# Performance work log

Measured on AMD Instinct MI355X. Metric: run time of the kernel, lower is better.

The kernel has to match this reference:

```python
import jax, jax.numpy as jnp
import numpy as np

C = 512        # num_channels
HEADS = 8      # num_channels // num_head_channels
DH = 64        # num_head_channels
G = 32         # num_groups
EPS = 1e-5
SCALE = DH ** -0.25  # pre-multiplied into q and k (scale applied twice -> 1/sqrt(DH))


def setup_inputs() -> dict:
    key = jax.random.key(0)
    ks = jax.random.split(key, 10)
    B, H, W = 2, 64, 64
    def w(k):
        return jax.random.normal(k, (C, C), jnp.float32) * 0.02
    def b(k):
        return jax.random.normal(k, (C,), jnp.float32) * 0.02
    return {
        "x": jax.random.normal(ks[0], (B, C, H, W), jnp.float32),
        "gn_w": jnp.ones((C,), jnp.float32),
        "gn_b": jnp.zeros((C,), jnp.float32),
        "wq": w(ks[1]), "bq": b(ks[2]),
        "wk": w(ks[3]), "bk": b(ks[4]),
        "wv": w(ks[5]), "bv": b(ks[6]),
        "wp": w(ks[7]), "bp": b(ks[8]),
    }


def reference(x, gn_w, gn_b, wq, bq, wk, bk, wv, bv, wp, bp):
    B, Cc, H, W = x.shape
    # GroupNorm over (C/G, H, W) per group
    xr = x.reshape(B, G, Cc // G, H * W)
    mean = xr.mean(axis=(2, 3), keepdims=True)
    var = xr.var(axis=(2, 3), keepdims=True)
    h = ((xr - mean) * jax.lax.rsqrt(var + EPS)).reshape(B, Cc, H, W)
    h = h * gn_w[None, :, None, None] + gn_b[None, :, None, None]
    # B C H W -> B (H W) C
    t = h.reshape(B, Cc, H * W).transpose(0, 2, 1)
    # q/k pre-multiplied by SCALE (equivalent to pre_multiply_weights_by_scale)
    q = (t @ wq.T + bq) * SCALE
    k = (t @ wk.T + bk) * SCALE
    v = t @ wv.T + bv
    def split_heads(a):  # B HW (h d) -> B h HW d
        return a.reshape(B, H * W, HEADS, DH).transpose(0, 2, 1, 3)
    q, k, v = split_heads(q), split_heads(k), split_heads(v)
    # full HWxHW score matrix, softmax over keys
    attn = jax.nn.softmax(jnp.einsum('bhqd,bhkd->bhqk', q, k), axis=-1)
    o = jnp.einsum('bhqk,bhkd->bhqd', attn, v)
    o = o.transpose(0, 2, 1, 3).reshape(B, H * W, Cc)  # join heads
    o = o @ wp.T + bp
    # B (H W) C -> B C H W, residual
    return o.transpose(0, 2, 1).reshape(B, Cc, H, W) + x
```

## Files before the change

### kernel.cpp

```cpp
#include <hip/hip_runtime.h>

#define HWN 4096
#define CCH 512
#define NHEAD 8
#define DHD 64
#define NBATCH 2
#define QK_SCALE 0.35355339059327373f
#define LOG2E    1.4426950408889634f

using floatx4 = __attribute__((ext_vector_type(4))) float;
using bf16x8  = __attribute__((ext_vector_type(8))) short;
using bf16x4  = __attribute__((ext_vector_type(4))) short;

__device__ __forceinline__ unsigned short f2b(float f) {
  union { float f; unsigned u; } x; x.f = f;
  unsigned r = x.u + 0x7FFFu + ((x.u >> 16) & 1u);
  return (unsigned short)(r >> 16);
}

__device__ __forceinline__ float b2f(unsigned short u) {
  union { unsigned u; float f; } x; x.u = ((unsigned)u) << 16;
  return x.f;
}

__device__ __forceinline__ float fast_exp2(float x) {
#if __has_builtin(__builtin_amdgcn_exp2f)
  return __builtin_amdgcn_exp2f(x);
#else
  return __expf(x * 0.69314718056f);
#endif
}

__device__ __forceinline__ unsigned pack_bf16_trunc(float lo, float hi) {
  return __builtin_amdgcn_perm(__float_as_uint(hi), __float_as_uint(lo), 0x07060302u);
}

__global__ __launch_bounds__(256) void prep_gn(
    const float* __restrict__ x, float* __restrict__ stat,
    const float* __restrict__ wq, const float* __restrict__ wk,
    const float* __restrict__ wv, const float* __restrict__ wp,
    const float* __restrict__ bq, const float* __restrict__ bk,
    const float* __restrict__ bv,
    unsigned short* __restrict__ Wqkv, unsigned short* __restrict__ Wp,
    float* __restrict__ bqkv) {
  if (blockIdx.x >= 4103) {
    int idx = blockIdx.x - 4103;
    int bg = idx & 63, part = idx >> 6;
    const float4* p = (const float4*)(x + (size_t)bg * 65536) + part * 2048;
    float s = 0.f, ss = 0.f;
    for (int i = threadIdx.x; i < 2048; i += 256) {
      float4 v = p[i];
      s  += v.x + v.y + v.z + v.w;
      ss += v.x*v.x + v.y*v.y + v.z*v.z + v.w*v.w;
    }
    for (int off = 32; off; off >>= 1) {
      s  += __shfl_xor(s, off);
      ss += __shfl_xor(ss, off);
    }
    __shared__ float red[8];
    int w = threadIdx.x >> 6;
    if ((threadIdx.x & 63) == 0) { red[w] = s; red[4 + w] = ss; }
    __syncthreads();
    if (threadIdx.x == 0) {
      float S  = red[0] + red[1] + red[2] + red[3];
      float SS = red[4] + red[5] + red[6] + red[7];
      atomicAdd(&stat[bg], S);
      atomicAdd(&stat[64 + bg], SS);
    }
    return;
  }
  int i = blockIdx.x * 256 + threadIdx.x;
  if (i < 786432) {
    int row = i >> 9;
    float v;
    if (row < 512)       v = wq[i] * (QK_SCALE * LOG2E);
    else if (row < 1024) v = wk[i - 262144] * QK_SCALE;
    else                 v = wv[i - 524288];
    Wqkv[i] = f2b(v);
  } else if (i < 1048576) {
    Wp[i - 786432] = f2b(wp[i - 786432]);
  } else if (i < 1050112) {
    int j = i - 1048576;
    float v = (j < 512) ? bq[j] * (QK_SCALE * LOG2E)
            : (j < 1024) ? bk[j - 512] * QK_SCALE
            : bv[j - 1024];
    bqkv[j] = v;
  }
}

__global__ __launch_bounds__(256) void gn_apply(
    const float* __restrict__ x, const float* __restrict__ stat,
    const float* __restrict__ gnw, const float* __restrict__ gnb,
    unsigned short* __restrict__ t) {
  int pt = blockIdx.x & 63;
  int ct = (blockIdx.x >> 6) & 7;
  int b  = blockIdx.x >> 9;
  int c0 = ct * 64, p0 = pt * 64;
  __shared__ float tile[64][68];
  int tid = threadIdx.x;
  for (int pp = 0; pp < 4; ++pp) {
    int f = (pp * 256 + tid) * 4;
    int cl = f >> 6, pl = f & 63;
    int c = c0 + cl;
    float4 v = *(const float4*)(x + ((size_t)(b * 512 + c)) * 4096 + p0 + pl);
    int g = c >> 4;
    float S    = stat[b * 32 + g];
    float SS   = stat[64 + b * 32 + g];
    float mean = S * (1.f / 65536.f);
    float var  = SS * (1.f / 65536.f) - mean * mean;
    float rstd = rsqrtf(var + 1e-5f);
    float w  = gnw[c] * rstd;
    float bb = gnb[c] - mean * w;
    tile[cl][pl + 0] = v.x * w + bb;
    tile[cl][pl + 1] = v.y * w + bb;
    tile[cl][pl + 2] = v.z * w + bb;
    tile[cl][pl + 3] = v.w * w + bb;
  }
  __syncthreads();
  for (int pp = 0; pp < 2; ++pp) {
    int f = (pp * 256 + tid) * 8;
    int pl = f >> 6, cl = f & 63;
    unsigned short u[8];
#pragma unroll
    for (int j = 0; j < 8; ++j) u[j] = f2b(tile[cl + j][pl]);
    *(uint4*)(t + ((size_t)(b * 4096 + p0 + pl)) * 512 + c0 + cl) = *(uint4*)u;
  }
}

__global__ __launch_bounds__(256) void gemm_qkv(
    const unsigned short* __restrict__ t, const unsigned short* __restrict__ Wqkv,
    const float* __restrict__ bqkv,
    unsigned short* __restrict__ qo, unsigned short* __restrict__ Kp,
    unsigned short* __restrict__ vo) {
  int M0 = blockIdx.x * 64;
  int N0 = blockIdx.y * 64;
  __shared__ unsigned short At[64][72];
  __shared__ unsigned short Bt[64][72];
  int tid = threadIdx.x, w = tid >> 6, l = tid & 63;
  int quad = l >> 4, m16 = l & 15;
  floatx4 acc[4] = {};
  for (int k0 = 0; k0 < 512; k0 += 64) {
    __syncthreads();
#pragma unroll
    for (int pp = 0; pp < 2; ++pp) {
      int f = (pp * 256 + tid) * 8;
      int r = f >> 6, c = f & 63;
      *(uint4*)&At[r][c] = *(const uint4*)(t    + (size_t)(M0 + r) * 512 + k0 + c);
      *(uint4*)&Bt[r][c] = *(const uint4*)(Wqkv + (size_t)(N0 + r) * 512 + k0 + c);
    }
    __syncthreads();
    bf16x8 af0 = *(const bf16x8*)&At[w * 16 + m16][quad * 8];
    bf16x8 af1 = *(const bf16x8*)&At[w * 16 + m16][32 + quad * 8];
#pragma unroll
    for (int nt = 0; nt < 4; ++nt) {
      bf16x8 b0 = *(const bf16x8*)&Bt[nt * 16 + m16][quad * 8];
      bf16x8 b1 = *(const bf16x8*)&Bt[nt * 16 + m16][32 + quad * 8];
      acc[nt] = __builtin_amdgcn_mfma_f32_16x16x32_bf16(af0, b0, acc[nt], 0, 0, 0);
      acc[nt] = __builtin_amdgcn_mfma_f32_16x16x32_bf16(af1, b1, acc[nt], 0, 0, 0);
    }
  }
  int which = N0 >> 9;
  int head  = (N0 & 511) >> 6;
  if (which == 2) {
    __syncthreads();
#pragma unroll
    for (int nt = 0; nt < 4; ++nt) {
      int d = nt * 16 + m16;
      float bias = bqkv[N0 + d];
#pragma unroll
      for (int r = 0; r < 4; ++r)
        At[d][w * 16 + quad * 4 + r] = f2b(acc[nt][r] + bias);
    }
    __syncthreads();
    int bb = M0 >> 12, p0 = M0 & 4095;
    unsigned short* dst = vo + ((size_t)(bb * 8 + head) * 64) * 4096;
#pragma unroll
    for (int pp = 0; pp < 2; ++pp) {
      int f = (pp * 256 + tid) * 8;
      int d = f >> 6, pl = f & 63;
      *(uint4*)(dst + (size_t)d * 4096 + p0 + pl) = *(uint4*)&At[d][pl];
    }
  } else if (which == 1) {
    __syncthreads();
#pragma unroll
    for (int nt = 0; nt < 4; ++nt) {
      float bias = bqkv[N0 + nt * 16 + m16];
#pragma unroll
      for (int r = 0; r < 4; ++r)
        At[w * 16 + quad * 4 + r][nt * 16 + m16] = f2b(acc[nt][r] + bias);
    }
    __syncthreads();
    int bb = M0 >> 12, p = M0 & 4095;
    int kb = p >> 7, halfblk = (p >> 6) & 1;
    int ig = halfblk * 4 + w;
    int ntl = w >> 1, hh = w & 1;
    int row = ntl * 32 + hh * 4 + ((m16 >> 2) << 3) + (m16 & 3);
    size_t dstb = (((size_t)(bb * 8 + head) * 32 + kb) * 8 + ig) * 1024;
#pragma unroll
    for (int pp = 0; pp < 2; ++pp)
      *(uint4*)(Kp + dstb + pp * 512 + l * 8) = *(uint4*)&At[row][pp * 32 + quad * 8];
  } else {
#pragma unroll
    for (int nt = 0; nt < 4; ++nt) {
      int n = N0 + nt * 16 + m16;
      float bias = bqkv[n];
      int d = n & 63;
#pragma unroll
      for (int r = 0; r < 4; ++r) {
        int m = M0 + w * 16 + quad * 4 + r;
        int b = m >> 12, pp2 = m & 4095;
        qo[(((size_t)(b * 8 + head) * 4096 + pp2) << 6) + d] = f2b(acc[nt][r] + bias);
      }
    }
  }
}

__global__ __launch_bounds__(256, 4) void attn(
    const unsigned short* __restrict__ q, const unsigned short* __restrict__ Kp,
    const unsigned short* __restrict__ vt,
    unsigned short* __restrict__ ob) {
  int qt = blockIdx.x;
  int bh = blockIdx.y;
  __shared__ unsigned short Klds[8192];
  __shared__ unsigned short Vt[64][128];
  int tid = threadIdx.x, w = tid >> 6, l = tid & 63;
  int quad = l >> 4, m16 = l & 15;
  const size_t vbase = (size_t)bh * HWN * DHD;

  int goff[4];
#pragma unroll
  for (int i = 0; i < 4; ++i) {
    int c = w * 4 + i;
    int row = 4 * c + (l >> 4);
    int cbl = l & 15;
    goff[i] = row * 4096 + ((cbl ^ (row & 15)) << 3);
  }

  bf16x8 qf0, qf1;
  {
    int qrow = qt * 64 + w * 16 + m16;
    const unsigned short* qp = q + vbase + (size_t)qrow * 64 + quad * 8;
    qf0 = *(const bf16x8*)qp;
    qf1 = *(const bf16x8*)(qp + 32);
  }
  bf16x8 ones;
#pragma unroll
  for (int z = 0; z < 8; ++z) ones[z] = (short)0x3F80;

  floatx4 accO[4] = {};
  floatx4 accL = {};
  float mrow = -1e30f;

  for (int kt = 0; kt < 32; ++kt) {
    __syncthreads();
    const unsigned short* kpb = Kp + (((size_t)bh * 32 + kt) * 8) * 1024;
    const unsigned short* vtile = vt + vbase + kt * 128;
#pragma unroll
    for (int i = 0; i < 4; ++i) {
      int c = w * 4 + i;
      __builtin_amdgcn_global_load_lds(
          (const __attribute__((address_space(1))) unsigned int*)(kpb + c * 512 + l * 8),
          (__attribute__((address_space(3))) unsigned int*)(Klds + c * 512),
          16, 0, 0);
      __builtin_amdgcn_global_load_lds(
          (const __attribute__((address_space(1))) unsigned int*)(vtile + goff[i]),
          (__attribute__((address_space(3))) unsigned int*)(&Vt[0][0] + c * 512),
          16, 0, 0);
    }
    __syncthreads();
    const unsigned short* kl = Klds + l * 8;
    floatx4 s[8];
#pragma unroll
    for (int ig = 0; ig < 8; ++ig) {
      bf16x8 kf0 = *(const bf16x8*)(kl + ig * 1024);
      bf16x8 kf1 = *(const bf16x8*)(kl + ig * 1024 + 512);
      floatx4 z = {};
      z = __builtin_amdgcn_mfma_f32_16x16x32_bf16(kf0, qf0, z, 0, 0, 0);
      s[ig] = __builtin_amdgcn_mfma_f32_16x16x32_bf16(kf1, qf1, z, 0, 0, 0);
    }
    float mx = s[0][0];
#pragma unroll
    for (int ig = 0; ig < 8; ++ig)
#pragma unroll
      for (int i = 0; i < 4; ++i) mx = fmaxf(mx, s[ig][i]);
    mx = fmaxf(mx, __shfl_xor(mx, 16));
    mx = fmaxf(mx, __shfl_xor(mx, 32));
    bool grew = mx > mrow + 8.0f;
    if (__ballot(grew)) {
      float mnew = grew ? mx : mrow;
      float alpha = fast_exp2(mrow - mnew);
      float al0 = __shfl(alpha, quad * 4 + 0);
      float al1 = __shfl(alpha, quad * 4 + 1);
      float al2 = __shfl(alpha, quad * 4 + 2);
      float al3 = __shfl(alpha, quad * 4 + 3);
#pragma unroll
      for (int dt = 0; dt < 4; ++dt) {
        accO[dt][0] *= al0; accO[dt][1] *= al1;
        accO[dt][2] *= al2; accO[dt][3] *= al3;
      }
      accL[0] *= al0; accL[1] *= al1; accL[2] *= al2; accL[3] *= al3;
      mrow = mnew;
    }
#pragma unroll
    for (int ig = 0; ig < 8; ++ig)
#pragma unroll
      for (int i = 0; i < 4; ++i)
        s[ig][i] = fast_exp2(s[ig][i] - mrow);
    bf16x8 pf[4];
#pragma unroll
    for (int nt = 0; nt < 4; ++nt) {
      union { unsigned u[4]; bf16x8 v; } pu;
      pu.u[0] = pack_bf16_trunc(s[nt * 2][0],     s[nt * 2][1]);
      pu.u[1] = pack_bf16_trunc(s[nt * 2][2],     s[nt * 2][3]);
      pu.u[2] = pack_bf16_trunc(s[nt * 2 + 1][0], s[nt * 2 + 1][1]);
      pu.u[3] = pack_bf16_trunc(s[nt * 2 + 1][2], s[nt * 2 + 1][3]);
      pf[nt] = pu.v;
    }
#pragma unroll
    for (int dt = 0; dt < 4; ++dt) {
#pragma unroll
      for (int nt = 0; nt < 4; ++nt) {
        bf16x8 vf = *(const bf16x8*)&Vt[dt * 16 + m16][((nt * 4 + quad) ^ m16) << 3];
        accO[dt] = __builtin_amdgcn_mfma_f32_16x16x32_bf16(pf[nt], vf, accO[dt], 0, 0, 0);
      }
    }
#pragma unroll
    for (int nt = 0; nt < 4; ++nt)
      accL = __builtin_amdgcn_mfma_f32_16x16x32_bf16(pf[nt], ones, accL, 0, 0, 0);
  }
  int b = bh >> 3, h = bh & 7;
  float li0 = 1.f / accL[0];
  float li1 = 1.f / accL[1];
  float li2 = 1.f / accL[2];
  float li3 = 1.f / accL[3];
  int qrow = qt * 64 + w * 16 + quad * 4;
  unsigned short* op = ob + ((size_t)(b * 4096 + qrow)) * 512 + h * 64;
#pragma unroll
  for (int dt = 0; dt < 4; ++dt) {
    int d = dt * 16 + m16;
    op[d]         = f2b(accO[dt][0] * li0);
    op[512 + d]   = f2b(accO[dt][1] * li1);
    op[1024 + d]  = f2b(accO[dt][2] * li2);
    op[1536 + d]  = f2b(accO[dt][3] * li3);
  }
}

__global__ __launch_bounds__(256) void gemm_out(
    const unsigned short* __restrict__ o, const unsigned short* __restrict__ Wp,
    const float* __restrict__ bp, const float* __restrict__ x,
    float* __restrict__ out) {
  int C0 = blockIdx.x * 64, P0 = blockIdx.y * 64, b = blockIdx.z;
  __shared__ unsigned short At[64][72];
  __shared__ unsigned short Bt[64][72];
  int tid = threadIdx.x, w = tid >> 6, l = tid & 63;
  int quad = l >> 4, m16 = l & 15;
  floatx4 acc[4] = {};
  for (int k0 = 0; k0 < 512; k0 += 64) {
    __syncthreads();
#pragma unroll
    for (int pp = 0; pp < 2; ++pp) {
      int f = (pp * 256 + tid) * 8;
      int r = f >> 6, c = f & 63;
      *(uint4*)&At[r][c] = *(const uint4*)(Wp + (size_t)(C0 + r) * 512 + k0 + c);
      *(uint4*)&Bt[r][c] = *(const uint4*)(o + ((size_t)(b * 4096 + P0 + r)) * 512 + k0 + c);
    }
    __syncthreads();
    bf16x8 af0 = *(const bf16x8*)&At[w * 16 + m16][quad * 8];
    bf16x8 af1 = *(const bf16x8*)&At[w * 16 + m16][32 + quad * 8];
#pragma unroll
    for (int nt = 0; nt < 4; ++nt) {
      bf16x8 b0 = *(const bf16x8*)&Bt[nt * 16 + m16][quad * 8];
      bf16x8 b1 = *(const bf16x8*)&Bt[nt * 16 + m16][32 + quad * 8];
      acc[nt] = __builtin_amdgcn_mfma_f32_16x16x32_bf16(af0, b0, acc[nt], 0, 0, 0);
      acc[nt] = __builtin_amdgcn_mfma_f32_16x16x32_bf16(af1, b1, acc[nt], 0, 0, 0);
    }
  }
#pragma unroll
  for (int r = 0; r < 4; ++r) {
    int c = C0 + w * 16 + quad * 4 + r;
    float bias = bp[c];
#pragma unroll
    for (int nt = 0; nt < 4; ++nt) {
      int p = P0 + nt * 16 + m16;
      size_t idx = ((size_t)(b * 512 + c)) * 4096 + p;
      out[idx] = acc[nt][r] + bias + x[idx];
    }
  }
}

extern "C" void kernel_launch(void* const* d_in, const int* in_sizes, int n_in,
                              void* d_out, int out_size, void* d_ws, size_t ws_size,
                              hipStream_t stream) {
  const float* x   = (const float*)d_in[0];
  const float* gnw = (const float*)d_in[1];
  const float* gnb = (const float*)d_in[2];
  const float* wq  = (const float*)d_in[3];
  const float* bq  = (const float*)d_in[4];
  const float* wk  = (const float*)d_in[5];
  const float* bk  = (const float*)d_in[6];
  const float* wv  = (const float*)d_in[7];
  const float* bv  = (const float*)d_in[8];
  const float* wp  = (const float*)d_in[9];
  const float* bp  = (const float*)d_in[10];
  float* out = (float*)d_out;

  char* ws = (char*)d_ws;
  float* stat          = (float*)ws;          ws += 1024;
  float* bqkv          = (float*)ws;          ws += 8192;
  unsigned short* Wqkv = (unsigned short*)ws; ws += (size_t)1536 * 512 * 2;
  unsigned short* Wp   = (unsigned short*)ws; ws += (size_t)512 * 512 * 2;
  unsigned short* t    = (unsigned short*)ws; ws += (size_t)8192 * 512 * 2;
  unsigned short* qb   = (unsigned short*)ws; ws += (size_t)8192 * 512 * 2;
  unsigned short* Kp   = (unsigned short*)ws; ws += (size_t)8192 * 512 * 2;
  unsigned short* vb   = (unsigned short*)ws; ws += (size_t)8192 * 512 * 2;
  unsigned short* ob   = (unsigned short*)ws; ws += (size_t)8192 * 512 * 2;

  hipMemsetAsync(stat, 0, 512, stream);
  prep_gn<<<4615, 256, 0, stream>>>(x, stat, wq, wk, wv, wp, bq, bk, bv, Wqkv, Wp, bqkv);
  gn_apply<<<1024, 256, 0, stream>>>(x, stat, gnw, gnb, t);
  dim3 g1(128, 24);
  gemm_qkv<<<g1, 256, 0, stream>>>(t, Wqkv, bqkv, qb, Kp, vb);
  dim3 g2(64, 16);
  attn<<<g2, 256, 0, stream>>>(qb, Kp, vb, ob);
  dim3 g3(8, 64, 2);
  gemm_out<<<g3, 256, 0, stream>>>(ob, Wp, bp, x, out);
}
```

Measured before the change: 229.4 us.

## Double-buffer K/V tiles in attention with 64-key tiles and prefetch

The attention loop now works on 64-key tiles instead of 128 and keeps two LDS buffers. The next K and V tile is loaded asynchronously while the current one is computed, so global load latency can overlap MFMA work and only one barrier is needed per iteration. The trade is twice as many iterations, each doing less work, which adds more online-softmax max/rescale steps and barriers. Total LDS use stays the same.

```diff
diff --git a/kernel.cpp b/kernel.cpp
--- a/kernel.cpp
+++ b/kernel.cpp
@@ -221,19 +221,20 @@
     unsigned short* __restrict__ ob) {
   int qt = blockIdx.x;
   int bh = blockIdx.y;
-  __shared__ unsigned short Klds[8192];
-  __shared__ unsigned short Vt[64][128];
+  __shared__ unsigned short Klds[2][4096];
+  __shared__ unsigned short Vt[2][64][64];
   int tid = threadIdx.x, w = tid >> 6, l = tid & 63;
   int quad = l >> 4, m16 = l & 15;
   const size_t vbase = (size_t)bh * HWN * DHD;
-
-  int goff[4];
-#pragma unroll
-  for (int i = 0; i < 4; ++i) {
-    int c = w * 4 + i;
-    int row = 4 * c + (l >> 4);
-    int cbl = l & 15;
-    goff[i] = row * 4096 + ((cbl ^ (row & 15)) << 3);
+  const unsigned short* kbase = Kp + (size_t)bh * 262144;
+
+  int vgoff[2];
+#pragma unroll
+  for (int i = 0; i < 2; ++i) {
+    int c = w * 2 + i;
+    int row = 8 * c + (l >> 3);
+    int cb = l & 7;
+    vgoff[i] = row * 4096 + ((cb ^ (row & 7)) << 3);
   }
 
   bf16x8 qf0, qf1;
@@ -251,27 +252,44 @@
   floatx4 accL = {};
   float mrow = -1e30f;
 
-  for (int kt = 0; kt < 32; ++kt) {
-    __syncthreads();
-    const unsigned short* kpb = Kp + (((size_t)bh * 32 + kt) * 8) * 1024;
-    const unsigned short* vtile = vt + vbase + kt * 128;
-#pragma unroll
-    for (int i = 0; i < 4; ++i) {
-      int c = w * 4 + i;
-      __builtin_amdgcn_global_load_lds(
-          (const __attribute__((address_space(1))) unsigned int*)(kpb + c * 512 + l * 8),
-          (__attribute__((address_space(3))) unsigned int*)(Klds + c * 512),
-          16, 0, 0);
-      __builtin_amdgcn_global_load_lds(
-          (const __attribute__((address_space(1))) unsigned int*)(vtile + goff[i]),
-          (__attribute__((address_space(3))) unsigned int*)(&Vt[0][0] + c * 512),
-          16, 0, 0);
-    }
-    __syncthreads();
-    const unsigned short* kl = Klds + l * 8;
-    floatx4 s[8];
-#pragma unroll
-    for (int ig = 0; ig < 8; ++ig) {
+#pragma unroll
+  for (int i = 0; i < 2; ++i) {
+    int c = w * 2 + i;
+    __builtin_amdgcn_global_load_lds(
+        (const __attribute__((address_space(1))) unsigned int*)(kbase + c * 512 + l * 8),
+        (__attribute__((address_space(3))) unsigned int*)(&Klds[0][0] + c * 512),
+        16, 0, 0);
+    __builtin_amdgcn_global_load_lds(
+        (const __attribute__((address_space(1))) unsigned int*)(vt + vbase + vgoff[i]),
+        (__attribute__((address_space(3))) unsigned int*)(&Vt[0][0][0] + c * 512),
+        16, 0, 0);
+  }
+  __syncthreads();
+
+  for (int kt = 0; kt < 64; ++kt) {
+    int cur = kt & 1;
+    if (kt < 63) {
+      const unsigned short* kpn = kbase + (kt + 1) * 4096;
+      const unsigned short* vpn = vt + vbase + (kt + 1) * 64;
+      unsigned short* kd = &Klds[cur ^ 1][0];
+      unsigned short* vd = &Vt[cur ^ 1][0][0];
+#pragma unroll
+      for (int i = 0; i < 2; ++i) {
+        int c = w * 2 + i;
+        __builtin_amdgcn_global_load_lds(
+            (const __attribute__((address_space(1))) unsigned int*)(kpn + c * 512 + l * 8),
+            (__attribute__((address_space(3))) unsigned int*)(kd + c * 512),
+            16, 0, 0);
+        __builtin_amdgcn_global_load_lds(
+            (const __attribute__((address_space(1))) unsigned int*)(vpn + vgoff[i]),
+            (__attribute__((address_space(3))) unsigned int*)(vd + c * 512),
+            16, 0, 0);
+      }
+    }
+    const unsigned short* kl = &Klds[cur][0] + l * 8;
+    floatx4 s[4];
+#pragma unroll
+    for (int ig = 0; ig < 4; ++ig) {
       bf16x8 kf0 = *(const bf16x8*)(kl + ig * 1024);
       bf16x8 kf1 = *(const bf16x8*)(kl + ig * 1024 + 512);
       floatx4 z = {};
@@ -280,7 +298,7 @@
     }
     float mx = s[0][0];
 #pragma unroll
-    for (int ig = 0; ig < 8; ++ig)
+    for (int ig = 0; ig < 4; ++ig)
 #pragma unroll
       for (int i = 0; i < 4; ++i) mx = fmaxf(mx, s[ig][i]);
     mx = fmaxf(mx, __shfl_xor(mx, 16));
@@ -302,13 +320,13 @@
       mrow = mnew;
     }
 #pragma unroll
-    for (int ig = 0; ig < 8; ++ig)
+    for (int ig = 0; ig < 4; ++ig)
 #pragma unroll
       for (int i = 0; i < 4; ++i)
         s[ig][i] = fast_exp2(s[ig][i] - mrow);
-    bf16x8 pf[4];
-#pragma unroll
-    for (int nt = 0; nt < 4; ++nt) {
+    bf16x8 pf[2];
+#pragma unroll
+    for (int nt = 0; nt < 2; ++nt) {
       union { unsigned u[4]; bf16x8 v; } pu;
       pu.u[0] = pack_bf16_trunc(s[nt * 2][0],     s[nt * 2][1]);
       pu.u[1] = pack_bf16_trunc(s[nt * 2][2],     s[nt * 2][3]);
@@ -319,14 +337,15 @@
 #pragma unroll
     for (int dt = 0; dt < 4; ++dt) {
 #pragma unroll
-      for (int nt = 0; nt < 4; ++nt) {
-        bf16x8 vf = *(const bf16x8*)&Vt[dt * 16 + m16][((nt * 4 + quad) ^ m16) << 3];
+      for (int nt = 0; nt < 2; ++nt) {
+        bf16x8 vf = *(const bf16x8*)&Vt[cur][dt * 16 + m16][((nt * 4 + quad) ^ (m16 & 7)) << 3];
         accO[dt] = __builtin_amdgcn_mfma_f32_16x16x32_bf16(pf[nt], vf, accO[dt], 0, 0, 0);
       }
     }
 #pragma unroll
-    for (int nt = 0; nt < 4; ++nt)
+    for (int nt = 0; nt < 2; ++nt)
       accL = __builtin_amdgcn_mfma_f32_16x16x32_bf16(pf[nt], ones, accL, 0, 0, 0);
+    __syncthreads();
   }
   int b = bh >> 3, h = bh & 7;
   float li0 = 1.f / accL[0];
```

New measurement: 237.5 us. +3.5%, slower.
